# Performance work log

Measured on AMD Instinct MI355X. Metric: run time of the kernel, lower is better.

Reference implementation:

```python
import jax, jax.numpy as jnp
import numpy as np

N_NODES = 50000
N_EDGES = 600000
IN_DIM, HID_DIM, OUT_DIM = 128, 256, 40


def setup_inputs() -> dict:
    key = jax.random.key(0)
    ks = jax.random.split(key, 10)
    x = jax.random.normal(ks[0], (N_NODES, IN_DIM), dtype=jnp.float32)
    edge_index = jax.random.randint(ks[1], (2, N_EDGES), 0, N_NODES, dtype=jnp.int64)
    def lin(k, out_d, in_d):
        s = 1.0 / np.sqrt(in_d)
        return jax.random.uniform(k, (out_d, in_d), jnp.float32, -s, s)
    # SAGEConv: lin_l (on aggregated neighbors, with bias) + lin_r (on self, no bias)
    params = {
        "Wl1": lin(ks[2], HID_DIM, IN_DIM), "bl1": jnp.zeros((HID_DIM,), jnp.float32), "Wr1": lin(ks[3], HID_DIM, IN_DIM),
        "Wl2": lin(ks[4], HID_DIM, HID_DIM), "bl2": jnp.zeros((HID_DIM,), jnp.float32), "Wr2": lin(ks[5], HID_DIM, HID_DIM),
        "Wl3": lin(ks[6], OUT_DIM, HID_DIM), "bl3": jnp.zeros((OUT_DIM,), jnp.float32), "Wr3": lin(ks[7], OUT_DIM, HID_DIM),
    }
    return {"x": x, "edge_index": edge_index, **params}


def _sage_conv(x, src, dst, Wl, bl, Wr):
    # mean-aggregate source features into destination nodes
    n = x.shape[0]
    agg = jax.ops.segment_sum(x[src], dst, num_segments=n)          # [N, d_in]
    cnt = jax.ops.segment_sum(jnp.ones_like(dst, dtype=x.dtype), dst, num_segments=n)
    mean = agg / jnp.maximum(cnt, 1.0)[:, None]
    return mean @ Wl.T + bl + x @ Wr.T


def reference(x, edge_index, Wl1, bl1, Wr1, Wl2, bl2, Wr2, Wl3, bl3, Wr3):
    src, dst = edge_index[0], edge_index[1]
    h = _sage_conv(x, src, dst, Wl1, bl1, Wr1)
    h = jax.nn.relu(h)  # dropout is identity in eval mode
    h = _sage_conv(h, src, dst, Wl2, bl2, Wr2)
    h = jax.nn.relu(h)
    h = _sage_conv(h, src, dst, Wl3, bl3, Wr3)
    return jax.nn.log_softmax(h, axis=1)
```

## Files before the change

kernel.cpp:

```cpp
#include <hip/hip_runtime.h>
#include <hip/hip_bf16.h>

#define IN_DIM 128
#define HID_DIM 256
#define OUT_DIM 40
#define SCAN_CHUNK 2048

typedef __attribute__((ext_vector_type(8))) __bf16 bf16x8;
typedef __attribute__((ext_vector_type(4))) float f32x4;

__device__ inline ushort f2bf(float f) {
    uint u = __builtin_bit_cast(uint, f);
    u = (u + 0x7fff + ((u >> 16) & 1)) >> 16;
    return (ushort)u;
}
__device__ inline float bfl(uint u) { return __builtin_bit_cast(float, u << 16); }
__device__ inline float bfh(uint u) { return __builtin_bit_cast(float, u & 0xffff0000u); }

__global__ __launch_bounds__(256) void cvt_x(const float* __restrict__ in,
                                             ushort* __restrict__ out, int n4) {
    int i = blockIdx.x * 256 + threadIdx.x;
    if (i < n4) {
        float4 v = ((const float4*)in)[i];
        uint2 o;
        o.x = (uint)f2bf(v.x) | ((uint)f2bf(v.y) << 16);
        o.y = (uint)f2bf(v.z) | ((uint)f2bf(v.w) << 16);
        ((uint2*)out)[i] = o;
    }
}

__global__ __launch_bounds__(256) void cvt_w2(const float* __restrict__ wl,
                                              const float* __restrict__ wr,
                                              ushort* __restrict__ ol,
                                              ushort* __restrict__ orr,
                                              int O, int OPAD, int K) {
    int idx = blockIdx.x * 256 + threadIdx.x;
    int tot = OPAD * K;
    if (idx >= tot) return;
    int row = idx / K;
    int col = idx - row * K;
    ushort vl = 0, vr = 0;
    if (row < O) {
        vl = f2bf(wl[row * K + col]);
        vr = f2bf(wr[row * K + col]);
    }
    ol[idx] = vl;
    orr[idx] = vr;
}

__global__ __launch_bounds__(256) void hist_kernel(const int* __restrict__ dst,
                                                   int* __restrict__ cnt, int E) {
    int e = blockIdx.x * 256 + threadIdx.x;
    if (e < E) atomicAdd(&cnt[dst[e]], 1);
}

__global__ __launch_bounds__(256) void scan_pass1(const int* __restrict__ cnt,
                                                  int* __restrict__ bsum, int N) {
    __shared__ int red[256];
    const int base = blockIdx.x * SCAN_CHUNK;
    int s = 0;
    for (int i = threadIdx.x; i < SCAN_CHUNK; i += 256) {
        int idx = base + i;
        if (idx < N) s += cnt[idx];
    }
    red[threadIdx.x] = s;
    __syncthreads();
    for (int o = 128; o > 0; o >>= 1) {
        if (threadIdx.x < o) red[threadIdx.x] += red[threadIdx.x + o];
        __syncthreads();
    }
    if (threadIdx.x == 0) bsum[blockIdx.x] = red[0];
}

__global__ __launch_bounds__(256) void scan_pass2(int* __restrict__ bsum, int B) {
    __shared__ int ls[256];
    const int t = threadIdx.x;
    int v = (t < B) ? bsum[t] : 0;
    ls[t] = v;
    __syncthreads();
    for (int o = 1; o < 256; o <<= 1) {
        int u = (t >= o) ? ls[t - o] : 0;
        __syncthreads();
        ls[t] += u;
        __syncthreads();
    }
    if (t < B) bsum[t] = ls[t] - v;
}

__global__ __launch_bounds__(256) void scan_pass3(const int* __restrict__ cnt,
                                                  const int* __restrict__ bsum,
                                                  int* __restrict__ rowptr,
                                                  int* __restrict__ cursor,
                                                  float* __restrict__ inv, int N, int E) {
    __shared__ int ls[256];
    const int tbase = blockIdx.x * SCAN_CHUNK + threadIdx.x * 8;
    int c[8];
    int s = 0;
#pragma unroll
    for (int j = 0; j < 8; ++j) {
        int idx = tbase + j;
        c[j] = (idx < N) ? cnt[idx] : 0;
        s += c[j];
    }
    ls[threadIdx.x] = s;
    __syncthreads();
    for (int o = 1; o < 256; o <<= 1) {
        int u = (threadIdx.x >= o) ? ls[threadIdx.x - o] : 0;
        __syncthreads();
        ls[threadIdx.x] += u;
        __syncthreads();
    }
    int run = bsum[blockIdx.x] + ls[threadIdx.x] - s;
#pragma unroll
    for (int j = 0; j < 8; ++j) {
        int idx = tbase + j;
        if (idx < N) {
            rowptr[idx] = run;
            cursor[idx] = run;
            inv[idx] = 1.0f / fmaxf((float)c[j], 1.0f);
            run += c[j];
        }
    }
    if (blockIdx.x == 0 && threadIdx.x == 0) rowptr[N] = E;
}

__global__ __launch_bounds__(256) void fill_kernel(const int* __restrict__ src,
                                                   const int* __restrict__ dst,
                                                   int* __restrict__ cursor,
                                                   int* __restrict__ srcs, int E) {
    int e = blockIdx.x * 256 + threadIdx.x;
    if (e < E) {
        int pos = atomicAdd(&cursor[dst[e]], 1);
        srcs[pos] = src[e];
    }
}

template <int D>
__global__ __launch_bounds__(256) void gather_mean_bf(const ushort* __restrict__ feat,
                                                      const int* __restrict__ rowptr,
                                                      const int* __restrict__ srcs,
                                                      const float* __restrict__ inv,
                                                      ushort* __restrict__ out, int N) {
    constexpr int V = D / 64;
    const int wave = threadIdx.x >> 6;
    const int lane = threadIdx.x & 63;
    const int n = blockIdx.x * 4 + wave;
    if (n >= N) return;
    const int beg = rowptr[n];
    const int end = rowptr[n + 1];
    const int col = lane * V;
    float a0 = 0.f, a1 = 0.f, a2 = 0.f, a3 = 0.f;
    int e = beg;
    if constexpr (V == 4) {
        for (; e + 3 < end; e += 4) {
            int s0 = srcs[e], s1 = srcs[e + 1], s2 = srcs[e + 2], s3 = srcs[e + 3];
            uint2 q0 = *(const uint2*)&feat[(long long)s0 * D + col];
            uint2 q1 = *(const uint2*)&feat[(long long)s1 * D + col];
            uint2 q2 = *(const uint2*)&feat[(long long)s2 * D + col];
            uint2 q3 = *(const uint2*)&feat[(long long)s3 * D + col];
            a0 += (bfl(q0.x) + bfl(q1.x)) + (bfl(q2.x) + bfl(q3.x));
            a1 += (bfh(q0.x) + bfh(q1.x)) + (bfh(q2.x) + bfh(q3.x));
            a2 += (bfl(q0.y) + bfl(q1.y)) + (bfl(q2.y) + bfl(q3.y));
            a3 += (bfh(q0.y) + bfh(q1.y)) + (bfh(q2.y) + bfh(q3.y));
        }
        for (; e + 1 < end; e += 2) {
            int s0 = srcs[e], s1 = srcs[e + 1];
            uint2 q0 = *(const uint2*)&feat[(long long)s0 * D + col];
            uint2 q1 = *(const uint2*)&feat[(long long)s1 * D + col];
            a0 += bfl(q0.x) + bfl(q1.x);
            a1 += bfh(q0.x) + bfh(q1.x);
            a2 += bfl(q0.y) + bfl(q1.y);
            a3 += bfh(q0.y) + bfh(q1.y);
        }
        if (e < end) {
            uint2 q0 = *(const uint2*)&feat[(long long)srcs[e] * D + col];
            a0 += bfl(q0.x); a1 += bfh(q0.x); a2 += bfl(q0.y); a3 += bfh(q0.y);
        }
        const float sc = inv[n];
        uint2 o;
        o.x = (uint)f2bf(a0 * sc) | ((uint)f2bf(a1 * sc) << 16);
        o.y = (uint)f2bf(a2 * sc) | ((uint)f2bf(a3 * sc) << 16);
        *(uint2*)&out[(long long)n * D + col] = o;
    } else {
        for (; e + 3 < end; e += 4) {
            int s0 = srcs[e], s1 = srcs[e + 1], s2 = srcs[e + 2], s3 = srcs[e + 3];
            uint q0 = *(const uint*)&feat[(long long)s0 * D + col];
            uint q1 = *(const uint*)&feat[(long long)s1 * D + col];
            uint q2 = *(const uint*)&feat[(long long)s2 * D + col];
            uint q3 = *(const uint*)&feat[(long long)s3 * D + col];
            a0 += (bfl(q0) + bfl(q1)) + (bfl(q2) + bfl(q3));
            a1 += (bfh(q0) + bfh(q1)) + (bfh(q2) + bfh(q3));
        }
        for (; e + 1 < end; e += 2) {
            int s0 = srcs[e], s1 = srcs[e + 1];
            uint q0 = *(const uint*)&feat[(long long)s0 * D + col];
            uint q1 = *(const uint*)&feat[(long long)s1 * D + col];
            a0 += bfl(q0) + bfl(q1);
            a1 += bfh(q0) + bfh(q1);
        }
        if (e < end) {
            uint q0 = *(const uint*)&feat[(long long)srcs[e] * D + col];
            a0 += bfl(q0); a1 += bfh(q0);
        }
        const float sc = inv[n];
        uint o = (uint)f2bf(a0 * sc) | ((uint)f2bf(a1 * sc) << 16);
        *(uint*)&out[(long long)n * D + col] = o;
    }
}

template <int K, bool RELU, bool OUTBF>
__global__ __launch_bounds__(256, 3) void sage_gemm_mfma(const ushort* __restrict__ Amean,
                                                         const ushort* __restrict__ Aself,
                                                         const ushort* __restrict__ Wl,
                                                         const float* __restrict__ bias,
                                                         const ushort* __restrict__ Wr,
                                                         void* __restrict__ outv, int N, int O) {
    constexpr int KP = K + 8;
    constexpr int NK = K / 32;
    __shared__ __align__(16) ushort Bs[64 * KP];

    const int tid = threadIdx.x;
    const int wave = tid >> 6;
    const int lane = tid & 63;
    const int ln = lane & 15;
    const int quad = lane >> 4;
    const int bm0 = blockIdx.x * 128;
    const int bn0 = blockIdx.y * 64;

    int arow[2];
#pragma unroll
    for (int rt = 0; rt < 2; ++rt) {
        int r = bm0 + wave * 32 + rt * 16 + ln;
        arow[rt] = min(r, N - 1);
    }

    f32x4 acc[2][4] = {};

    for (int phase = 0; phase < 2; ++phase) {
        const ushort* __restrict__ A = phase ? Aself : Amean;
        const ushort* __restrict__ W = phase ? Wr : Wl;

        bf16x8 areg[NK][2];
#pragma unroll
        for (int kk = 0; kk < NK; ++kk)
#pragma unroll
            for (int rt = 0; rt < 2; ++rt)
                areg[kk][rt] = *(const bf16x8*)&A[(long long)arow[rt] * K + kk * 32 + quad * 8];

        __syncthreads();
#pragma unroll
        for (int i = tid; i < 64 * (K / 8); i += 256) {
            int row = i / (K / 8);
            int c8 = (i % (K / 8)) * 8;
            *(ulonglong2*)&Bs[row * KP + c8] =
                *(const ulonglong2*)&W[(long long)(bn0 + row) * K + c8];
        }
        __syncthreads();

#pragma unroll
        for (int kk = 0; kk < NK; ++kk) {
#pragma unroll
            for (int ct = 0; ct < 4; ++ct) {
                bf16x8 b = *(const bf16x8*)&Bs[(ct * 16 + ln) * KP + kk * 32 + quad * 8];
#pragma unroll
                for (int rt = 0; rt < 2; ++rt)
                    acc[rt][ct] = __builtin_amdgcn_mfma_f32_16x16x32_bf16(areg[kk][rt], b, acc[rt][ct], 0, 0, 0);
            }
        }
    }

#pragma unroll
    for (int rt = 0; rt < 2; ++rt) {
        int rbase = bm0 + wave * 32 + rt * 16 + quad * 4;
#pragma unroll
        for (int ct = 0; ct < 4; ++ct) {
            int col = bn0 + ct * 16 + ln;
            if (col >= O) continue;
            float bv = bias[col];
#pragma unroll
            for (int r = 0; r < 4; ++r) {
                int row = rbase + r;
                if (row >= N) continue;
                float v = acc[rt][ct][r] + bv;
                if (RELU) v = fmaxf(v, 0.f);
                if (OUTBF)
                    ((ushort*)outv)[(long long)row * O + col] = f2bf(v);
                else
                    ((float*)outv)[(long long)row * O + col] = v;
            }
        }
    }
}

template <int K>
__global__ __launch_bounds__(256, 3) void sage_gemm_pre(const ushort* __restrict__ A0,
                                                        const ushort* __restrict__ Wl,
                                                        const ushort* __restrict__ Wr,
                                                        ushort* __restrict__ P,
                                                        float* __restrict__ S, int N, int O) {
    constexpr int KP = K + 8;
    constexpr int NK = K / 32;
    __shared__ __align__(16) ushort Bs[64 * KP];

    const int tid = threadIdx.x;
    const int wave = tid >> 6;
    const int lane = tid & 63;
    const int ln = lane & 15;
    const int quad = lane >> 4;
    const int bm0 = blockIdx.x * 128;

    int arow[2];
#pragma unroll
    for (int rt = 0; rt < 2; ++rt) {
        int r = bm0 + wave * 32 + rt * 16 + ln;
        arow[rt] = min(r, N - 1);
    }

    bf16x8 areg[NK][2];
#pragma unroll
    for (int kk = 0; kk < NK; ++kk)
#pragma unroll
        for (int rt = 0; rt < 2; ++rt)
            areg[kk][rt] = *(const bf16x8*)&A0[(long long)arow[rt] * K + kk * 32 + quad * 8];

    for (int phase = 0; phase < 2; ++phase) {
        const ushort* __restrict__ W = phase ? Wr : Wl;

        __syncthreads();
#pragma unroll
        for (int i = tid; i < 64 * (K / 8); i += 256) {
            int row = i / (K / 8);
            int c8 = (i % (K / 8)) * 8;
            *(ulonglong2*)&Bs[row * KP + c8] =
                *(const ulonglong2*)&W[(long long)row * K + c8];
        }
        __syncthreads();

        f32x4 acc[2][4] = {};
#pragma unroll
        for (int kk = 0; kk < NK; ++kk) {
#pragma unroll
            for (int ct = 0; ct < 4; ++ct) {
                bf16x8 b = *(const bf16x8*)&Bs[(ct * 16 + ln) * KP + kk * 32 + quad * 8];
#pragma unroll
                for (int rt = 0; rt < 2; ++rt)
                    acc[rt][ct] = __builtin_amdgcn_mfma_f32_16x16x32_bf16(areg[kk][rt], b, acc[rt][ct], 0, 0, 0);
            }
        }

#pragma unroll
        for (int rt = 0; rt < 2; ++rt) {
            int rbase = bm0 + wave * 32 + rt * 16 + quad * 4;
#pragma unroll
            for (int ct = 0; ct < 3; ++ct) {
                int col = ct * 16 + ln;
                if (col >= O) continue;
#pragma unroll
                for (int r = 0; r < 4; ++r) {
                    int row = rbase + r;
                    if (row >= N) continue;
                    if (phase == 0)
                        P[(long long)row * O + col] = f2bf(acc[rt][ct][r]);
                    else
                        S[(long long)row * O + col] = acc[rt][ct][r];
                }
            }
        }
    }
}

__global__ __launch_bounds__(256) void agg_bias_lsm(const ushort* __restrict__ P,
                                                    const float* __restrict__ S,
                                                    const float* __restrict__ bias,
                                                    const int* __restrict__ rowptr,
                                                    const int* __restrict__ srcs,
                                                    const float* __restrict__ inv,
                                                    float* __restrict__ out, int N) {
    const int wave = threadIdx.x >> 6;
    const int lane = threadIdx.x & 63;
    const int n = blockIdx.x * 4 + wave;
    if (n >= N) return;
    const int beg = rowptr[n];
    const int end = rowptr[n + 1];
    const bool act = lane < OUT_DIM;
    const int cidx = act ? lane : 0;

    float acc = 0.f;
    int e = beg;
    for (; e + 3 < end; e += 4) {
        int s0 = srcs[e], s1 = srcs[e + 1], s2 = srcs[e + 2], s3 = srcs[e + 3];
        float v0 = __builtin_bit_cast(float, (uint)P[(long long)s0 * OUT_DIM + cidx] << 16);
        float v1 = __builtin_bit_cast(float, (uint)P[(long long)s1 * OUT_DIM + cidx] << 16);
        float v2 = __builtin_bit_cast(float, (uint)P[(long long)s2 * OUT_DIM + cidx] << 16);
        float v3 = __builtin_bit_cast(float, (uint)P[(long long)s3 * OUT_DIM + cidx] << 16);
        acc += (v0 + v1) + (v2 + v3);
    }
    for (; e < end; ++e)
        acc += __builtin_bit_cast(float, (uint)P[(long long)srcs[e] * OUT_DIM + cidx] << 16);

    float v = act ? (acc * inv[n] + S[(long long)n * OUT_DIM + lane] + bias[lane]) : -INFINITY;
    float m = v;
#pragma unroll
    for (int o = 32; o > 0; o >>= 1) m = fmaxf(m, __shfl_xor(m, o, 64));
    float ex = act ? expf(v - m) : 0.f;
    float sm = ex;
#pragma unroll
    for (int o = 32; o > 0; o >>= 1) sm += __shfl_xor(sm, o, 64);
    float ls = logf(sm);
    if (act) out[(long long)n * OUT_DIM + lane] = v - m - ls;
}

extern "C" void kernel_launch(void* const* d_in, const int* in_sizes, int n_in,
                              void* d_out, int out_size, void* d_ws, size_t ws_size,
                              hipStream_t stream) {
    const float* x   = (const float*)d_in[0];
    const int*   ei  = (const int*)d_in[1];
    const float* Wl1 = (const float*)d_in[2];
    const float* bl1 = (const float*)d_in[3];
    const float* Wr1 = (const float*)d_in[4];
    const float* Wl2 = (const float*)d_in[5];
    const float* bl2 = (const float*)d_in[6];
    const float* Wr2 = (const float*)d_in[7];
    const float* Wl3 = (const float*)d_in[8];
    const float* bl3 = (const float*)d_in[9];
    const float* Wr3 = (const float*)d_in[10];
    float* out = (float*)d_out;

    const int N = in_sizes[0] / IN_DIM;
    const int E = in_sizes[1] / 2;
    const int* src = ei;
    const int* dst = ei + E;

    char* w = (char*)d_ws;
    size_t off = 0;
    auto alloc = [&](size_t bytes) {
        void* p = w + off;
        off = (off + bytes + 255) & ~(size_t)255;
        return p;
    };
    ushort* xb   = (ushort*)alloc((size_t)N * IN_DIM * 2);
    ushort* M    = (ushort*)alloc((size_t)N * HID_DIM * 2);
    ushort* H1   = (ushort*)alloc((size_t)N * HID_DIM * 2);
    ushort* H2   = (ushort*)alloc((size_t)N * HID_DIM * 2);
    ushort* P3   = (ushort*)alloc((size_t)N * OUT_DIM * 2);
    float*  S3   = (float*)alloc((size_t)N * OUT_DIM * 4);
    float*  inv  = (float*)alloc((size_t)N * 4);
    int*    cnt  = (int*)alloc((size_t)N * 4);
    int*    rowptr = (int*)alloc((size_t)(N + 1) * 4);
    int*    cursor = (int*)alloc((size_t)N * 4);
    int*    srcs = (int*)alloc((size_t)E * 4);
    int*    bsum = (int*)alloc(256 * 4);
    ushort* Wl1b = (ushort*)alloc(256 * 128 * 2);
    ushort* Wr1b = (ushort*)alloc(256 * 128 * 2);
    ushort* Wl2b = (ushort*)alloc(256 * 256 * 2);
    ushort* Wr2b = (ushort*)alloc(256 * 256 * 2);
    ushort* Wl3b = (ushort*)alloc(64 * 256 * 2);
    ushort* Wr3b = (ushort*)alloc(64 * 256 * 2);

    cvt_x<<<(N * IN_DIM / 4 + 255) / 256, 256, 0, stream>>>(x, xb, N * IN_DIM / 4);
    cvt_w2<<<(256 * 128 + 255) / 256, 256, 0, stream>>>(Wl1, Wr1, Wl1b, Wr1b, 256, 256, 128);
    cvt_w2<<<(256 * 256 + 255) / 256, 256, 0, stream>>>(Wl2, Wr2, Wl2b, Wr2b, 256, 256, 256);
    cvt_w2<<<(64 * 256 + 255) / 256, 256, 0, stream>>>(Wl3, Wr3, Wl3b, Wr3b, 40, 64, 256);

    const int SB = (N + SCAN_CHUNK - 1) / SCAN_CHUNK;
    hipMemsetAsync(cnt, 0, (size_t)N * sizeof(int), stream);
    hist_kernel<<<(E + 255) / 256, 256, 0, stream>>>(dst, cnt, E);
    scan_pass1<<<SB, 256, 0, stream>>>(cnt, bsum, N);
    scan_pass2<<<1, 256, 0, stream>>>(bsum, SB);
    scan_pass3<<<SB, 256, 0, stream>>>(cnt, bsum, rowptr, cursor, inv, N, E);
    fill_kernel<<<(E + 255) / 256, 256, 0, stream>>>(src, dst, cursor, srcs, E);

    const int gm = (N + 127) / 128;
    const int gg = (N + 3) / 4;

    gather_mean_bf<IN_DIM><<<gg, 256, 0, stream>>>(xb, rowptr, srcs, inv, M, N);
    sage_gemm_mfma<IN_DIM, true, true><<<dim3(gm, 4), 256, 0, stream>>>(
        M, xb, Wl1b, bl1, Wr1b, H1, N, HID_DIM);

    gather_mean_bf<HID_DIM><<<gg, 256, 0, stream>>>(H1, rowptr, srcs, inv, M, N);
    sage_gemm_mfma<HID_DIM, true, true><<<dim3(gm, 4), 256, 0, stream>>>(
        M, H1, Wl2b, bl2, Wr2b, H2, N, HID_DIM);

    sage_gemm_pre<HID_DIM><<<dim3(gm, 1), 256, 0, stream>>>(
        H2, Wl3b, Wr3b, P3, S3, N, OUT_DIM);
    agg_bias_lsm<<<gg, 256, 0, stream>>>(P3, S3, bl3, rowptr, srcs, inv, out, N);
}
```

Before: 372.0 us.

## Stage concatenated Wl|Wr weights once and software-pipeline A-fragment loads in SAGE GEMMs

The hidden-layer GEMM now loads both Wl and Wr tiles into one shared-memory buffer up front. It treats the two products as a single K=2K reduction and streams A fragments with a one-step register prefetch, which removes the mid-kernel barrier and the bulk A register preload. Blocks are laid out on a 1D grid with the column tile in the low bits, so the four column blocks of a row tile run close together and can share A in cache. The final-layer pre-GEMM uses 64-row tiles and loads both weights once with a single sync. The larger shared-memory footprint lowers the launch_bounds occupancy hint from 3 to 2.

```diff
diff --git a/kernel.cpp b/kernel.cpp
--- a/kernel.cpp
+++ b/kernel.cpp
@@ -209,23 +209,24 @@
 }
 
 template <int K, bool RELU, bool OUTBF>
-__global__ __launch_bounds__(256, 3) void sage_gemm_mfma(const ushort* __restrict__ Amean,
-                                                         const ushort* __restrict__ Aself,
-                                                         const ushort* __restrict__ Wl,
-                                                         const float* __restrict__ bias,
-                                                         const ushort* __restrict__ Wr,
-                                                         void* __restrict__ outv, int N, int O) {
-    constexpr int KP = K + 8;
-    constexpr int NK = K / 32;
-    __shared__ __align__(16) ushort Bs[64 * KP];
+__global__ __launch_bounds__(256, 2) void sage_gemm_fused(const ushort* __restrict__ Amean,
+                                                          const ushort* __restrict__ Aself,
+                                                          const ushort* __restrict__ Wl,
+                                                          const float* __restrict__ bias,
+                                                          const ushort* __restrict__ Wr,
+                                                          void* __restrict__ outv, int N, int O) {
+    constexpr int K2 = 2 * K;
+    constexpr int KP = K2 + 8;
+    constexpr int NK = K2 / 32;
+    __shared__ __align__(16) ushort Ws[64 * KP];
 
     const int tid = threadIdx.x;
     const int wave = tid >> 6;
     const int lane = tid & 63;
     const int ln = lane & 15;
     const int quad = lane >> 4;
-    const int bm0 = blockIdx.x * 128;
-    const int bn0 = blockIdx.y * 64;
+    const int bm0 = (blockIdx.x >> 2) * 128;
+    const int bn0 = (blockIdx.x & 3) * 64;
 
     int arow[2];
 #pragma unroll
@@ -234,39 +235,42 @@
         arow[rt] = min(r, N - 1);
     }
 
+#pragma unroll
+    for (int i = tid; i < 64 * (K / 8); i += 256) {
+        int row = i / (K / 8);
+        int c8 = (i % (K / 8)) * 8;
+        *(ulonglong2*)&Ws[row * KP + c8] =
+            *(const ulonglong2*)&Wl[(long long)(bn0 + row) * K + c8];
+        *(ulonglong2*)&Ws[row * KP + K + c8] =
+            *(const ulonglong2*)&Wr[(long long)(bn0 + row) * K + c8];
+    }
+
     f32x4 acc[2][4] = {};
-
-    for (int phase = 0; phase < 2; ++phase) {
-        const ushort* __restrict__ A = phase ? Aself : Amean;
-        const ushort* __restrict__ W = phase ? Wr : Wl;
-
-        bf16x8 areg[NK][2];
-#pragma unroll
-        for (int kk = 0; kk < NK; ++kk)
+    bf16x8 a_cur[2], a_nxt[2];
+#pragma unroll
+    for (int rt = 0; rt < 2; ++rt)
+        a_cur[rt] = *(const bf16x8*)&Amean[(long long)arow[rt] * K + quad * 8];
+
+    __syncthreads();
+
+#pragma unroll
+    for (int kk = 0; kk < NK; ++kk) {
+        if (kk + 1 < NK) {
+            const ushort* __restrict__ An = (kk + 1 < NK / 2) ? Amean : Aself;
+            const int ko = ((kk + 1) % (NK / 2)) * 32;
 #pragma unroll
             for (int rt = 0; rt < 2; ++rt)
-                areg[kk][rt] = *(const bf16x8*)&A[(long long)arow[rt] * K + kk * 32 + quad * 8];
-
-        __syncthreads();
-#pragma unroll
-        for (int i = tid; i < 64 * (K / 8); i += 256) {
-            int row = i / (K / 8);
-            int c8 = (i % (K / 8)) * 8;
-            *(ulonglong2*)&Bs[row * KP + c8] =
-                *(const ulonglong2*)&W[(long long)(bn0 + row) * K + c8];
-        }
-        __syncthreads();
-
-#pragma unroll
-        for (int kk = 0; kk < NK; ++kk) {
-#pragma unroll
-            for (int ct = 0; ct < 4; ++ct) {
-                bf16x8 b = *(const bf16x8*)&Bs[(ct * 16 + ln) * KP + kk * 32 + quad * 8];
-#pragma unroll
-                for (int rt = 0; rt < 2; ++rt)
-                    acc[rt][ct] = __builtin_amdgcn_mfma_f32_16x16x32_bf16(areg[kk][rt], b, acc[rt][ct], 0, 0, 0);
-            }
-        }
+                a_nxt[rt] = *(const bf16x8*)&An[(long long)arow[rt] * K + ko + quad * 8];
+        }
+#pragma unroll
+        for (int ct = 0; ct < 4; ++ct) {
+            bf16x8 b = *(const bf16x8*)&Ws[(ct * 16 + ln) * KP + kk * 32 + quad * 8];
+#pragma unroll
+            for (int rt = 0; rt < 2; ++rt)
+                acc[rt][ct] = __builtin_amdgcn_mfma_f32_16x16x32_bf16(a_cur[rt], b, acc[rt][ct], 0, 0, 0);
+        }
+#pragma unroll
+        for (int rt = 0; rt < 2; ++rt) a_cur[rt] = a_nxt[rt];
     }
 
 #pragma unroll
@@ -293,77 +297,64 @@
 }
 
 template <int K>
-__global__ __launch_bounds__(256, 3) void sage_gemm_pre(const ushort* __restrict__ A0,
+__global__ __launch_bounds__(256, 2) void sage_gemm_pre(const ushort* __restrict__ A0,
                                                         const ushort* __restrict__ Wl,
                                                         const ushort* __restrict__ Wr,
                                                         ushort* __restrict__ P,
                                                         float* __restrict__ S, int N, int O) {
-    constexpr int KP = K + 8;
+    constexpr int KP = 2 * K + 8;
     constexpr int NK = K / 32;
-    __shared__ __align__(16) ushort Bs[64 * KP];
+    __shared__ __align__(16) ushort Ws[64 * KP];
 
     const int tid = threadIdx.x;
     const int wave = tid >> 6;
     const int lane = tid & 63;
     const int ln = lane & 15;
     const int quad = lane >> 4;
-    const int bm0 = blockIdx.x * 128;
-
-    int arow[2];
-#pragma unroll
-    for (int rt = 0; rt < 2; ++rt) {
-        int r = bm0 + wave * 32 + rt * 16 + ln;
-        arow[rt] = min(r, N - 1);
-    }
-
-    bf16x8 areg[NK][2];
+    const int bm0 = blockIdx.x * 64;
+
+    const int arow = min(bm0 + wave * 16 + ln, N - 1);
+
+    bf16x8 areg[NK];
 #pragma unroll
     for (int kk = 0; kk < NK; ++kk)
-#pragma unroll
-        for (int rt = 0; rt < 2; ++rt)
-            areg[kk][rt] = *(const bf16x8*)&A0[(long long)arow[rt] * K + kk * 32 + quad * 8];
-
+        areg[kk] = *(const bf16x8*)&A0[(long long)arow * K + kk * 32 + quad * 8];
+
+#pragma unroll
+    for (int i = tid; i < 64 * (K / 8); i += 256) {
+        int row = i / (K / 8);
+        int c8 = (i % (K / 8)) * 8;
+        *(ulonglong2*)&Ws[row * KP + c8] =
+            *(const ulonglong2*)&Wl[(long long)row * K + c8];
+        *(ulonglong2*)&Ws[row * KP + K + c8] =
+            *(const ulonglong2*)&Wr[(long long)row * K + c8];
+    }
+    __syncthreads();
+
+#pragma unroll
     for (int phase = 0; phase < 2; ++phase) {
-        const ushort* __restrict__ W = phase ? Wr : Wl;
-
-        __syncthreads();
-#pragma unroll
-        for (int i = tid; i < 64 * (K / 8); i += 256) {
-            int row = i / (K / 8);
-            int c8 = (i % (K / 8)) * 8;
-            *(ulonglong2*)&Bs[row * KP + c8] =
-                *(const ulonglong2*)&W[(long long)row * K + c8];
-        }
-        __syncthreads();
-
-        f32x4 acc[2][4] = {};
+        f32x4 acc[4] = {};
 #pragma unroll
         for (int kk = 0; kk < NK; ++kk) {
 #pragma unroll
             for (int ct = 0; ct < 4; ++ct) {
-                bf16x8 b = *(const bf16x8*)&Bs[(ct * 16 + ln) * KP + kk * 32 + quad * 8];
-#pragma unroll
-                for (int rt = 0; rt < 2; ++rt)
-                    acc[rt][ct] = __builtin_amdgcn_mfma_f32_16x16x32_bf16(areg[kk][rt], b, acc[rt][ct], 0, 0, 0);
+                bf16x8 b = *(const bf16x8*)&Ws[(ct * 16 + ln) * KP + phase * K + kk * 32 + quad * 8];
+                acc[ct] = __builtin_amdgcn_mfma_f32_16x16x32_bf16(areg[kk], b, acc[ct], 0, 0, 0);
             }
         }
-
-#pragma unroll
-        for (int rt = 0; rt < 2; ++rt) {
-            int rbase = bm0 + wave * 32 + rt * 16 + quad * 4;
-#pragma unroll
-            for (int ct = 0; ct < 3; ++ct) {
-                int col = ct * 16 + ln;
-                if (col >= O) continue;
-#pragma unroll
-                for (int r = 0; r < 4; ++r) {
-                    int row = rbase + r;
-                    if (row >= N) continue;
-                    if (phase == 0)
-                        P[(long long)row * O + col] = f2bf(acc[rt][ct][r]);
-                    else
-                        S[(long long)row * O + col] = acc[rt][ct][r];
-                }
+        int rbase = bm0 + wave * 16 + quad * 4;
+#pragma unroll
+        for (int ct = 0; ct < 3; ++ct) {
+            int col = ct * 16 + ln;
+            if (col >= O) continue;
+#pragma unroll
+            for (int r = 0; r < 4; ++r) {
+                int row = rbase + r;
+                if (row >= N) continue;
+                if (phase == 0)
+                    P[(long long)row * O + col] = f2bf(acc[ct][r]);
+                else
+                    S[(long long)row * O + col] = acc[ct][r];
             }
         }
     }
@@ -474,14 +465,14 @@
     const int gg = (N + 3) / 4;
 
     gather_mean_bf<IN_DIM><<<gg, 256, 0, stream>>>(xb, rowptr, srcs, inv, M, N);
-    sage_gemm_mfma<IN_DIM, true, true><<<dim3(gm, 4), 256, 0, stream>>>(
+    sage_gemm_fused<IN_DIM, true, true><<<gm * 4, 256, 0, stream>>>(
         M, xb, Wl1b, bl1, Wr1b, H1, N, HID_DIM);
 
     gather_mean_bf<HID_DIM><<<gg, 256, 0, stream>>>(H1, rowptr, srcs, inv, M, N);
-    sage_gemm_mfma<HID_DIM, true, true><<<dim3(gm, 4), 256, 0, stream>>>(
+    sage_gemm_fused<HID_DIM, true, true><<<gm * 4, 256, 0, stream>>>(
         M, H1, Wl2b, bl2, Wr2b, H2, N, HID_DIM);
 
-    sage_gemm_pre<HID_DIM><<<dim3(gm, 1), 256, 0, stream>>>(
+    sage_gemm_pre<HID_DIM><<<(N + 63) / 64, 256, 0, stream>>>(
         H2, Wl3b, Wr3b, P3, S3, N, OUT_DIM);
     agg_bias_lsm<<<gg, 256, 0, stream>>>(P3, S3, bl3, rowptr, srcs, inv, out, N);
 }
```

Result: slower. 381.0 us (+2.4%).
